# Kernel optimization log

Measured on AMD Instinct MI355X. Metric: run time of the kernel, lower is better.

Reference implementation:

```python
import jax, jax.numpy as jnp
import numpy as np

IN_CH, OUT_CH, HEAD, QK_DIM, V_DIM = 256, 256, 8, 512, 512


def setup_inputs() -> dict:
    key = jax.random.key(0)
    ks = jax.random.split(key, 5)
    B, H, W = 16, 32, 32
    x = jax.random.normal(ks[0], (B, IN_CH, H, W), dtype=jnp.float32)
    # 1x1 conv weights stored as [out_ch, in_ch]
    qkv_out = 2 * QK_DIM + V_DIM
    qkv_w = jax.random.normal(ks[1], (qkv_out, IN_CH), dtype=jnp.float32) * (IN_CH ** -0.5)
    qkv_b = jax.random.normal(ks[2], (qkv_out,), dtype=jnp.float32) * 0.02
    proj_w = jax.random.normal(ks[3], (OUT_CH, V_DIM), dtype=jnp.float32) * (V_DIM ** -0.5)
    proj_b = jax.random.normal(ks[4], (OUT_CH,), dtype=jnp.float32) * 0.02
    return {"x": x, "qkv_w": qkv_w, "qkv_b": qkv_b, "proj_w": proj_w, "proj_b": proj_b}


def reference(x, qkv_w, qkv_b, proj_w, proj_b):
    B, C, H, W = x.shape
    N = H * W
    dh = QK_DIM // HEAD
    dv = V_DIM // HEAD
    scale = dh ** -0.5
    # 1x1 conv == channel GEMM
    qkv = jnp.einsum('bchw,oc->bohw', x, qkv_w) + qkv_b[None, :, None, None]
    q, k, v = jnp.split(qkv, [QK_DIM, 2 * QK_DIM], axis=1)
    # [B, ch, H, W] -> [B, head, N, head_dim]
    def to_heads(t, d):
        return t.reshape(B, HEAD, d, N).transpose(0, 1, 3, 2)
    q = to_heads(q, dh)
    k = to_heads(k, dh)
    v = to_heads(v, dv)
    mask = jnp.tril(jnp.ones((N, N), dtype=bool))  # [N, N]
    scores = jnp.einsum('bhnd,bhmd->bhnm', q, k) * scale
    scores = jnp.where(mask, scores, -jnp.inf)
    attn = jax.nn.softmax(scores, axis=-1)
    attn = jnp.where(mask, attn, 0.0)
    out = jnp.einsum('bhnm,bhmd->bhnd', attn, v)  # [B, head, N, dv]
    out = out.transpose(0, 1, 3, 2).reshape(B, V_DIM, H, W)
    out = jnp.einsum('bvhw,ov->bohw', out, proj_w) + proj_b[None, :, None, None]
    return out
```

## Files before the change

### kernel.cpp

```cpp
#include <hip/hip_runtime.h>
#include <math.h>

static constexpr int Bsz = 16;
static constexpr int Np  = 1024;
static constexpr int Cin = 256;

typedef __attribute__((ext_vector_type(8))) short short8;
typedef __attribute__((ext_vector_type(4))) float f4;

#if defined(__has_builtin)
#if __has_builtin(__builtin_amdgcn_exp2f)
#define EXP2(x) __builtin_amdgcn_exp2f(x)
#else
#define EXP2(x) exp2f(x)
#endif
#else
#define EXP2(x) exp2f(x)
#endif

#define QSCALE 0.18033688011112f

__device__ __forceinline__ unsigned short f2b(float f) {
    union { float fp; unsigned int u; } v; v.fp = f;
    unsigned int r = v.u + 0x7fffu + ((v.u >> 16) & 1u);
    return (unsigned short)(r >> 16);
}

__device__ __forceinline__ unsigned cvtpk(float a, float b) {
    unsigned r;
    asm("v_cvt_pk_bf16_f32 %0, %1, %2" : "=v"(r) : "v"(a), "v"(b));
    return r;
}

__device__ __forceinline__ void* swzp(const void* base, int row, int col) {
    return (void*)((const char*)base + ((row * 128 + col * 2) ^ ((row & 7) << 4)));
}

__global__ __launch_bounds__(256)
void cast_xw(const float* __restrict__ x, const float* __restrict__ qw,
             const float* __restrict__ pw, ushort* __restrict__ xb,
             ushort* __restrict__ qwb, ushort* __restrict__ pwb)
{
    const int t = threadIdx.x;
    if (blockIdx.y < 4) {
        __shared__ ushort T[64][72];
        const int n0 = blockIdx.x * 64, c0 = blockIdx.y * 64, b = blockIdx.z;
        {
            const int c_l = t >> 2, ns = (t & 3) * 16;
            const float* src = &x[((b * Cin + c0 + c_l) << 10) + n0 + ns];
#pragma unroll
            for (int i = 0; i < 4; ++i) {
                const float4 v = *(const float4*)(src + 4 * i);
                T[ns + 4 * i + 0][c_l] = f2b(v.x);
                T[ns + 4 * i + 1][c_l] = f2b(v.y);
                T[ns + 4 * i + 2][c_l] = f2b(v.z);
                T[ns + 4 * i + 3][c_l] = f2b(v.w);
            }
        }
        __syncthreads();
        {
            const int n_l = t >> 2, cs = (t & 3) * 16;
            ushort* dst = &xb[((b << 10) + n0 + n_l) * Cin + c0 + cs];
            *(uint4*)dst       = *(const uint4*)&T[n_l][cs];
            *(uint4*)(dst + 8) = *(const uint4*)&T[n_l][cs + 8];
        }
    } else {
        const int nq4 = (1536 * Cin) / 4;
        const int base = ((blockIdx.z * 16 + blockIdx.x) * 256 + t) * 2;
#pragma unroll
        for (int g = 0; g < 2; ++g) {
            const int j = base + g;
            const float* src; ushort* dst; int jj;
            if (j < nq4) { src = qw; dst = qwb; jj = j; }
            else         { src = pw; dst = pwb; jj = j - nq4; }
            const float4 v = *(const float4*)(src + 4 * jj);
            ushort4 u; u.x = f2b(v.x); u.y = f2b(v.y); u.z = f2b(v.z); u.w = f2b(v.w);
            *(ushort4*)(dst + 4 * jj) = u;
        }
    }
}

__global__ __launch_bounds__(256)
void qkv_gemm(const ushort* __restrict__ xb, const ushort* __restrict__ wb,
              const float* __restrict__ bias,
              ushort* __restrict__ qb, ushort* __restrict__ kb, ushort* __restrict__ vb)
{
    __shared__ ushort lds[18432];
    ushort* As = lds;
    ushort* Bs = lds + 9216;

    const int t = threadIdx.x;
    const int w = t >> 6, lane = t & 63, quad = lane >> 4, ln = lane & 15;
    const int n0 = blockIdx.x * 128;
    const int o0 = blockIdx.y * 128;
    const int b  = blockIdx.z;
    const int ow = (w & 1) * 64, nw = (w >> 1) * 64;
    const bool vpath = (o0 >= 1024);

    f4 acc[4][4];
#pragma unroll
    for (int i = 0; i < 4; ++i)
#pragma unroll
        for (int j = 0; j < 4; ++j) acc[i][j] = (f4){0.f, 0.f, 0.f, 0.f};

    const int rr = t >> 2, cc = (t & 3) * 16;
    for (int k0 = 0; k0 < Cin; k0 += 64) {
        __syncthreads();
#pragma unroll
        for (int p = 0; p < 2; ++p) {
            const int row = rr + p * 64;
            const ushort* sa = &wb[(o0 + row) * Cin + k0 + cc];
            *(uint4*)&As[row * 72 + cc]     = *(const uint4*)sa;
            *(uint4*)&As[row * 72 + cc + 8] = *(const uint4*)(sa + 8);
            const ushort* sb = &xb[((b << 10) + n0 + row) * Cin + k0 + cc];
            *(uint4*)&Bs[row * 72 + cc]     = *(const uint4*)sb;
            *(uint4*)&Bs[row * 72 + cc + 8] = *(const uint4*)(sb + 8);
        }
        __syncthreads();
#pragma unroll
        for (int sub = 0; sub < 2; ++sub) {
            short8 af[4], bf[4];
#pragma unroll
            for (int ot = 0; ot < 4; ++ot)
                af[ot] = *(const short8*)&As[(ow + ot * 16 + ln) * 72 + sub * 32 + quad * 8];
#pragma unroll
            for (int nt = 0; nt < 4; ++nt)
                bf[nt] = *(const short8*)&Bs[(nw + nt * 16 + ln) * 72 + sub * 32 + quad * 8];
            if (!vpath) {
#pragma unroll
                for (int ot = 0; ot < 4; ++ot)
#pragma unroll
                    for (int nt = 0; nt < 4; ++nt)
                        acc[ot][nt] = __builtin_amdgcn_mfma_f32_16x16x32_bf16(
                            af[ot], bf[nt], acc[ot][nt], 0, 0, 0);
            } else {
#pragma unroll
                for (int nt = 0; nt < 4; ++nt)
#pragma unroll
                    for (int ot = 0; ot < 4; ++ot)
                        acc[nt][ot] = __builtin_amdgcn_mfma_f32_16x16x32_bf16(
                            bf[nt], af[ot], acc[nt][ot], 0, 0, 0);
            }
        }
    }

    __syncthreads();
    if (!vpath) {
        ushort* Ct = lds;
        const float sc = (o0 < 512) ? QSCALE : 1.0f;
#pragma unroll
        for (int ot = 0; ot < 4; ++ot) {
            float bs[4];
#pragma unroll
            for (int rg = 0; rg < 4; ++rg)
                bs[rg] = bias[o0 + ow + ot * 16 + quad * 4 + rg];
#pragma unroll
            for (int nt = 0; nt < 4; ++nt) {
                ushort4 u;
                u.x = f2b((acc[ot][nt][0] + bs[0]) * sc);
                u.y = f2b((acc[ot][nt][1] + bs[1]) * sc);
                u.z = f2b((acc[ot][nt][2] + bs[2]) * sc);
                u.w = f2b((acc[ot][nt][3] + bs[3]) * sc);
                *(ushort4*)&Ct[(nw + nt * 16 + ln) * 136 + ow + ot * 16 + quad * 4] = u;
            }
        }
        __syncthreads();
        ushort* dst; int obase;
        if (o0 < 512) { dst = qb; obase = o0; }
        else          { dst = kb; obase = o0 - 512; }
        const int rn = t >> 1, hf = t & 1;
        const int bh = b * 8 + (obase >> 6) + hf;
        ushort* drow = &dst[(bh * Np + n0 + rn) << 6];
        const ushort* srow = &Ct[rn * 136 + hf * 64];
#pragma unroll
        for (int s = 0; s < 8; ++s)
            *(uint4*)(drow + s * 8) = *(const uint4*)(srow + s * 8);
    } else {
        ushort* Ct = lds;
#pragma unroll
        for (int ot = 0; ot < 4; ++ot) {
            const float bo = bias[o0 + ow + ot * 16 + ln];
#pragma unroll
            for (int nt = 0; nt < 4; ++nt) {
                ushort4 u;
                u.x = f2b(acc[nt][ot][0] + bo);
                u.y = f2b(acc[nt][ot][1] + bo);
                u.z = f2b(acc[nt][ot][2] + bo);
                u.w = f2b(acc[nt][ot][3] + bo);
                *(ushort4*)&Ct[(ow + ot * 16 + ln) * 136 + nw + nt * 16 + quad * 4] = u;
            }
        }
        __syncthreads();
        const int o_l = t >> 1, nh = (t & 1) * 64;
        const int bh = b * 8 + ((o0 - 1024) >> 6) + (o_l >> 6);
        ushort* drow = &vb[((size_t)bh << 16) + ((o_l & 63) << 10) + n0 + nh];
        const ushort* srow = &Ct[o_l * 136 + nh];
#pragma unroll
        for (int s = 0; s < 8; ++s)
            *(uint4*)(drow + s * 8) = *(const uint4*)(srow + s * 8);
    }
}

__global__ __launch_bounds__(256, 6)
void attn(const ushort* __restrict__ qb, const ushort* __restrict__ kb,
          const ushort* __restrict__ vt, ushort* __restrict__ ob)
{
    __shared__ ushort Ks[64 * 64];
    __shared__ ushort Vt[64 * 64];
    __shared__ ushort Ps[64 * 72];

    const int t    = threadIdx.x;
    const int w    = t >> 6;
    const int lane = t & 63;
    const int quad = lane >> 4;
    const int ln   = lane & 15;
    const int bh   = blockIdx.x & 127;
    const int qt   = 15 - (int)(blockIdx.x >> 7);
    const int q0   = qt * 64;

    const ushort* __restrict__ kbh = kb + ((size_t)(bh * Np) << 6);
    const ushort* __restrict__ vbh = vt + ((size_t)bh << 16);

    {
        const int r = t & 63, seg = t >> 6;
        const ushort* src = &qb[((size_t)(bh * Np + q0 + r) << 6) + seg * 16];
        *(uint4*)&Ps[r * 72 + seg * 16]     = *(const uint4*)src;
        *(uint4*)&Ps[r * 72 + seg * 16 + 8] = *(const uint4*)(src + 8);
    }
    __syncthreads();

    const short8 qa0 = *(const short8*)&Ps[(w * 16 + ln) * 72 + quad * 8];
    const short8 qa1 = *(const short8*)&Ps[(w * 16 + ln) * 72 + 32 + quad * 8];

    f4 o_[4];
#pragma unroll
    for (int nt = 0; nt < 4; ++nt) o_[nt] = (f4){0.f, 0.f, 0.f, 0.f};
    float m = -INFINITY, l = 0.f;

    const int srow = t >> 2, scol = (t & 3) * 16;
    const int prow = (w * 16 + ln) * 72;
    const int qrow = q0 + w * 16 + ln;

    for (int kt = 0; kt <= qt; ++kt) {
        const int k0 = kt * 64;
        __syncthreads();
        {
            const ushort* sk = &kbh[((k0 + srow) << 6) + scol];
            *(uint4*)swzp(Ks, srow, scol)     = *(const uint4*)sk;
            *(uint4*)swzp(Ks, srow, scol + 8) = *(const uint4*)(sk + 8);
            const ushort* sv = &vbh[(srow << 10) + k0 + scol];
            *(uint4*)swzp(Vt, srow, scol)     = *(const uint4*)sv;
            *(uint4*)swzp(Vt, srow, scol + 8) = *(const uint4*)(sv + 8);
        }
        __syncthreads();

        const bool diag = (kt == qt);

        f4 st[4];
#pragma unroll
        for (int mt = 0; mt < 4; ++mt) st[mt] = (f4){0.f, 0.f, 0.f, 0.f};
#pragma unroll
        for (int mt = 0; mt < 4; ++mt) {
            if (diag && mt > w) continue;
            const short8 ka0 = *(const short8*)swzp(Ks, mt * 16 + ln, quad * 8);
            const short8 ka1 = *(const short8*)swzp(Ks, mt * 16 + ln, 32 + quad * 8);
            st[mt] = __builtin_amdgcn_mfma_f32_16x16x32_bf16(ka0, qa0, st[mt], 0, 0, 0);
            st[mt] = __builtin_amdgcn_mfma_f32_16x16x32_bf16(ka1, qa1, st[mt], 0, 0, 0);
        }

        if (diag) {
#pragma unroll
            for (int mt = 0; mt < 4; ++mt)
#pragma unroll
                for (int rg = 0; rg < 4; ++rg)
                    if (k0 + mt * 16 + quad * 4 + rg > qrow) st[mt][rg] = -INFINITY;
        }

        float mx = st[0][0];
#pragma unroll
        for (int mt = 0; mt < 4; ++mt)
#pragma unroll
            for (int rg = 0; rg < 4; ++rg) mx = fmaxf(mx, st[mt][rg]);
        mx = fmaxf(mx, __shfl_xor(mx, 16));
        mx = fmaxf(mx, __shfl_xor(mx, 32));

        if (!__all(mx <= m + 8.f)) {
            const float mn = fmaxf(m, mx);
            const float al = EXP2(m - mn);
            m = mn; l *= al;
#pragma unroll
            for (int nt = 0; nt < 4; ++nt)
#pragma unroll
                for (int rg = 0; rg < 4; ++rg) o_[nt][rg] *= al;
        }

        float rs = 0.f;
#pragma unroll
        for (int mt = 0; mt < 4; ++mt) {
            const float p0 = EXP2(st[mt][0] - m);
            const float p1 = EXP2(st[mt][1] - m);
            const float p2 = EXP2(st[mt][2] - m);
            const float p3 = EXP2(st[mt][3] - m);
            rs += (p0 + p1) + (p2 + p3);
            uint2 u; u.x = cvtpk(p0, p1); u.y = cvtpk(p2, p3);
            *(uint2*)&Ps[prow + mt * 16 + quad * 4] = u;
        }
        rs += __shfl_xor(rs, 16);
        rs += __shfl_xor(rs, 32);
        l += rs;

#pragma unroll
        for (int ks = 0; ks < 2; ++ks) {
            if (diag && w * 16 + 15 < ks * 32) continue;
            const short8 pa = *(const short8*)&Ps[prow + ks * 32 + quad * 8];
#pragma unroll
            for (int nt = 0; nt < 4; ++nt) {
                const short8 vf = *(const short8*)swzp(Vt, nt * 16 + ln, ks * 32 + quad * 8);
                o_[nt] = __builtin_amdgcn_mfma_f32_16x16x32_bf16(vf, pa, o_[nt], 0, 0, 0);
            }
        }
    }

    const float li = 1.0f / l;
    ushort* orow = &ob[(size_t)(bh * Np + qrow) << 6];
#pragma unroll
    for (int nt = 0; nt < 4; ++nt) {
        uint2 u;
        u.x = cvtpk(o_[nt][0] * li, o_[nt][1] * li);
        u.y = cvtpk(o_[nt][2] * li, o_[nt][3] * li);
        *(uint2*)(orow + nt * 16 + quad * 4) = u;
    }
}

__global__ __launch_bounds__(256)
void proj_gemm(const ushort* __restrict__ obuf, const ushort* __restrict__ pwb,
               const float* __restrict__ bias, float* __restrict__ out)
{
    __shared__ ushort As[64 * 72];
    __shared__ ushort Bs[128 * 72];

    const int t = threadIdx.x;
    const int w = t >> 6, lane = t & 63, quad = lane >> 4, ln = lane & 15;
    const int n0 = blockIdx.x * 128;
    const int o0 = blockIdx.y * 64;
    const int b  = blockIdx.z;
    const int nw = w * 32;

    f4 acc[4][2];
#pragma unroll
    for (int i = 0; i < 4; ++i)
#pragma unroll
        for (int j = 0; j < 2; ++j) acc[i][j] = (f4){0.f, 0.f, 0.f, 0.f};

    const int rr = t >> 2, cc = (t & 3) * 16;
    for (int k0 = 0; k0 < 512; k0 += 64) {
        __syncthreads();
        {
            const ushort* sa = &pwb[(o0 + rr) * 512 + k0 + cc];
            *(uint4*)&As[rr * 72 + cc]     = *(const uint4*)sa;
            *(uint4*)&As[rr * 72 + cc + 8] = *(const uint4*)(sa + 8);
            const int head = k0 >> 6;
#pragma unroll
            for (int p = 0; p < 2; ++p) {
                const int row = rr + p * 64;
                const ushort* sb = &obuf[(((b * 8 + head) * Np + n0 + row) << 6) + cc];
                *(uint4*)&Bs[row * 72 + cc]     = *(const uint4*)sb;
                *(uint4*)&Bs[row * 72 + cc + 8] = *(const uint4*)(sb + 8);
            }
        }
        __syncthreads();
#pragma unroll
        for (int sub = 0; sub < 2; ++sub) {
            short8 af[4], bf[2];
#pragma unroll
            for (int ot = 0; ot < 4; ++ot)
                af[ot] = *(const short8*)&As[(ot * 16 + ln) * 72 + sub * 32 + quad * 8];
#pragma unroll
            for (int nt = 0; nt < 2; ++nt)
                bf[nt] = *(const short8*)&Bs[(nw + nt * 16 + ln) * 72 + sub * 32 + quad * 8];
#pragma unroll
            for (int ot = 0; ot < 4; ++ot)
#pragma unroll
                for (int nt = 0; nt < 2; ++nt)
                    acc[ot][nt] = __builtin_amdgcn_mfma_f32_16x16x32_bf16(
                        af[ot], bf[nt], acc[ot][nt], 0, 0, 0);
        }
    }

#pragma unroll
    for (int ot = 0; ot < 4; ++ot) {
#pragma unroll
        for (int rg = 0; rg < 4; ++rg) {
            const int oo = o0 + ot * 16 + quad * 4 + rg;
            const float pb = bias[oo];
            float* drow = &out[((b << 8) + oo) << 10];
#pragma unroll
            for (int nt = 0; nt < 2; ++nt)
                drow[n0 + nw + nt * 16 + ln] = acc[ot][nt][rg] + pb;
        }
    }
}

extern "C" void kernel_launch(void* const* d_in, const int* in_sizes, int n_in,
                              void* d_out, int out_size, void* d_ws, size_t ws_size,
                              hipStream_t stream)
{
    const float* x   = (const float*)d_in[0];
    const float* qw  = (const float*)d_in[1];
    const float* qbb = (const float*)d_in[2];
    const float* pw  = (const float*)d_in[3];
    const float* pb  = (const float*)d_in[4];
    float* out = (float*)d_out;

    const size_t per = (size_t)Bsz * 8 * Np * 64;
    ushort* qbuf = (ushort*)d_ws;
    ushort* kbuf = qbuf + per;
    ushort* vbuf = kbuf + per;
    ushort* obuf = vbuf + per;
    ushort* xb   = obuf + per;
    ushort* qwb  = xb + (size_t)Bsz * Np * Cin;
    ushort* pwb  = qwb + 1536 * Cin;

    cast_xw<<<dim3(16, 5, Bsz), 256, 0, stream>>>(x, qw, pw, xb, qwb, pwb);
    qkv_gemm<<<dim3(8, 12, Bsz), 256, 0, stream>>>(xb, qwb, qbb, qbuf, kbuf, vbuf);
    attn<<<dim3(128 * 16), 256, 0, stream>>>(qbuf, kbuf, vbuf, obuf);
    proj_gemm<<<dim3(8, 4, Bsz), 256, 0, stream>>>(obuf, pwb, pb, out);
}
```

Measured before the change: 152.3 us.

## Load GEMM and attention tiles directly into LDS via global_load_lds

```diff
diff --git a/kernel.cpp b/kernel.cpp
--- a/kernel.cpp
+++ b/kernel.cpp
@@ -34,6 +34,12 @@
 
 __device__ __forceinline__ void* swzp(const void* base, int row, int col) {
     return (void*)((const char*)base + ((row * 128 + col * 2) ^ ((row & 7) << 4)));
+}
+
+__device__ __forceinline__ void gl16(const ushort* g, ushort* l) {
+    __builtin_amdgcn_global_load_lds(
+        (const __attribute__((address_space(1))) unsigned int*)g,
+        (__attribute__((address_space(3))) unsigned int*)l, 16, 0, 0);
 }
 
 __global__ __launch_bounds__(256)
@@ -85,9 +91,9 @@
               const float* __restrict__ bias,
               ushort* __restrict__ qb, ushort* __restrict__ kb, ushort* __restrict__ vb)
 {
-    __shared__ ushort lds[18432];
+    __shared__ ushort lds[17408];
     ushort* As = lds;
-    ushort* Bs = lds + 9216;
+    ushort* Bs = lds + 8192;
 
     const int t = threadIdx.x;
     const int w = t >> 6, lane = t & 63, quad = lane >> 4, ln = lane & 15;
@@ -97,24 +103,22 @@
     const int ow = (w & 1) * 64, nw = (w >> 1) * 64;
     const bool vpath = (o0 >= 1024);
 
+    const int r8  = lane >> 3;
+    const int c16 = ((lane & 7) ^ r8) << 3;
+
     f4 acc[4][4];
 #pragma unroll
     for (int i = 0; i < 4; ++i)
 #pragma unroll
         for (int j = 0; j < 4; ++j) acc[i][j] = (f4){0.f, 0.f, 0.f, 0.f};
 
-    const int rr = t >> 2, cc = (t & 3) * 16;
     for (int k0 = 0; k0 < Cin; k0 += 64) {
         __syncthreads();
 #pragma unroll
-        for (int p = 0; p < 2; ++p) {
-            const int row = rr + p * 64;
-            const ushort* sa = &wb[(o0 + row) * Cin + k0 + cc];
-            *(uint4*)&As[row * 72 + cc]     = *(const uint4*)sa;
-            *(uint4*)&As[row * 72 + cc + 8] = *(const uint4*)(sa + 8);
-            const ushort* sb = &xb[((b << 10) + n0 + row) * Cin + k0 + cc];
-            *(uint4*)&Bs[row * 72 + cc]     = *(const uint4*)sb;
-            *(uint4*)&Bs[row * 72 + cc + 8] = *(const uint4*)(sb + 8);
+        for (int j = 0; j < 4; ++j) {
+            const int row = w * 32 + j * 8 + r8;
+            gl16(&wb[(o0 + row) * Cin + k0 + c16],              &As[(w * 32 + j * 8) * 64]);
+            gl16(&xb[((b << 10) + n0 + row) * Cin + k0 + c16],  &Bs[(w * 32 + j * 8) * 64]);
         }
         __syncthreads();
 #pragma unroll
@@ -122,10 +126,10 @@
             short8 af[4], bf[4];
 #pragma unroll
             for (int ot = 0; ot < 4; ++ot)
-                af[ot] = *(const short8*)&As[(ow + ot * 16 + ln) * 72 + sub * 32 + quad * 8];
+                af[ot] = *(const short8*)swzp(As, ow + ot * 16 + ln, sub * 32 + quad * 8);
 #pragma unroll
             for (int nt = 0; nt < 4; ++nt)
-                bf[nt] = *(const short8*)&Bs[(nw + nt * 16 + ln) * 72 + sub * 32 + quad * 8];
+                bf[nt] = *(const short8*)swzp(Bs, nw + nt * 16 + ln, sub * 32 + quad * 8);
             if (!vpath) {
 #pragma unroll
                 for (int ot = 0; ot < 4; ++ot)
@@ -237,20 +241,20 @@
     for (int nt = 0; nt < 4; ++nt) o_[nt] = (f4){0.f, 0.f, 0.f, 0.f};
     float m = -INFINITY, l = 0.f;
 
-    const int srow = t >> 2, scol = (t & 3) * 16;
+    const int r8  = lane >> 3;
+    const int c16 = ((lane & 7) ^ r8) << 3;
     const int prow = (w * 16 + ln) * 72;
     const int qrow = q0 + w * 16 + ln;
 
     for (int kt = 0; kt <= qt; ++kt) {
         const int k0 = kt * 64;
         __syncthreads();
-        {
-            const ushort* sk = &kbh[((k0 + srow) << 6) + scol];
-            *(uint4*)swzp(Ks, srow, scol)     = *(const uint4*)sk;
-            *(uint4*)swzp(Ks, srow, scol + 8) = *(const uint4*)(sk + 8);
-            const ushort* sv = &vbh[(srow << 10) + k0 + scol];
-            *(uint4*)swzp(Vt, srow, scol)     = *(const uint4*)sv;
-            *(uint4*)swzp(Vt, srow, scol + 8) = *(const uint4*)(sv + 8);
+#pragma unroll
+        for (int j = 0; j < 2; ++j) {
+            const int ch  = w * 2 + j;
+            const int row = ch * 8 + r8;
+            gl16(&kbh[((k0 + row) << 6) + c16],               &Ks[ch * 512]);
+            gl16(&vbh[((size_t)row << 10) + k0 + c16],        &Vt[ch * 512]);
         }
         __syncthreads();
 
@@ -336,8 +340,8 @@
 void proj_gemm(const ushort* __restrict__ obuf, const ushort* __restrict__ pwb,
                const float* __restrict__ bias, float* __restrict__ out)
 {
-    __shared__ ushort As[64 * 72];
-    __shared__ ushort Bs[128 * 72];
+    __shared__ ushort As[64 * 64];
+    __shared__ ushort Bs[128 * 64];
 
     const int t = threadIdx.x;
     const int w = t >> 6, lane = t & 63, quad = lane >> 4, ln = lane & 15;
@@ -346,26 +350,28 @@
     const int b  = blockIdx.z;
     const int nw = w * 32;
 
+    const int r8  = lane >> 3;
+    const int c16 = ((lane & 7) ^ r8) << 3;
+
     f4 acc[4][2];
 #pragma unroll
     for (int i = 0; i < 4; ++i)
 #pragma unroll
         for (int j = 0; j < 2; ++j) acc[i][j] = (f4){0.f, 0.f, 0.f, 0.f};
 
-    const int rr = t >> 2, cc = (t & 3) * 16;
     for (int k0 = 0; k0 < 512; k0 += 64) {
         __syncthreads();
         {
-            const ushort* sa = &pwb[(o0 + rr) * 512 + k0 + cc];
-            *(uint4*)&As[rr * 72 + cc]     = *(const uint4*)sa;
-            *(uint4*)&As[rr * 72 + cc + 8] = *(const uint4*)(sa + 8);
             const int head = k0 >> 6;
 #pragma unroll
-            for (int p = 0; p < 2; ++p) {
-                const int row = rr + p * 64;
-                const ushort* sb = &obuf[(((b * 8 + head) * Np + n0 + row) << 6) + cc];
-                *(uint4*)&Bs[row * 72 + cc]     = *(const uint4*)sb;
-                *(uint4*)&Bs[row * 72 + cc + 8] = *(const uint4*)(sb + 8);
+            for (int j = 0; j < 2; ++j) {
+                const int ch = w * 2 + j, row = ch * 8 + r8;
+                gl16(&pwb[(o0 + row) * 512 + k0 + c16], &As[ch * 512]);
+            }
+#pragma unroll
+            for (int j = 0; j < 4; ++j) {
+                const int ch = w * 4 + j, row = ch * 8 + r8;
+                gl16(&obuf[(((b * 8 + head) * Np + n0 + row) << 6) + c16], &Bs[ch * 512]);
             }
         }
         __syncthreads();
@@ -374,10 +380,10 @@
             short8 af[4], bf[2];
 #pragma unroll
             for (int ot = 0; ot < 4; ++ot)
-                af[ot] = *(const short8*)&As[(ot * 16 + ln) * 72 + sub * 32 + quad * 8];
+                af[ot] = *(const short8*)swzp(As, ot * 16 + ln, sub * 32 + quad * 8);
 #pragma unroll
             for (int nt = 0; nt < 2; ++nt)
-                bf[nt] = *(const short8*)&Bs[(nw + nt * 16 + ln) * 72 + sub * 32 + quad * 8];
+                bf[nt] = *(const short8*)swzp(Bs, nw + nt * 16 + ln, sub * 32 + quad * 8);
 #pragma unroll
             for (int ot = 0; ot < 4; ++ot)
 #pragma unroll
```

Result: no change. 151.2 us (median of 2 runs) (-0.7%).
